# Optimization experiments

Hardware: AMD Instinct MI355X
Metric: run time of the kernel (lower is better)

The kernel has to match this reference:

```python
import jax, jax.numpy as jnp
import numpy as np

N_NODES = 10000
N_EDGES = 640000
D_FEAT = 128


def setup_inputs() -> dict:
    key = jax.random.key(0)
    k1, k2, k3 = jax.random.split(key, 3)
    feat = jax.random.normal(k1, (N_NODES, D_FEAT), dtype=jnp.float32)
    src = jax.random.randint(k2, (N_EDGES,), 0, N_NODES, dtype=jnp.int64)
    dst = jax.random.randint(k3, (N_EDGES,), 0, N_NODES, dtype=jnp.int64)
    beta = jnp.ones((1,), dtype=jnp.float32)
    return {"feat": feat, "src": src, "dst": dst, "beta": beta}


def reference(feat, src, dst, beta):
    # L2-normalize node features along feature dim (eps matches torch F.normalize)
    norm = feat / jnp.maximum(jnp.linalg.norm(feat, axis=-1, keepdims=True), 1e-12)
    # per-edge cosine similarity: sum over d of norm[src] * norm[dst]  -> [E]
    cos = jnp.einsum('ed,ed->e', norm[src], norm[dst])
    e = beta[0] * cos
    # edge softmax segmented over destination nodes
    seg_max = jax.ops.segment_max(e, dst, num_segments=N_NODES)  # [N]
    ex = jnp.exp(e - seg_max[dst])                               # [E]
    seg_sum = jax.ops.segment_sum(ex, dst, num_segments=N_NODES)  # [N]
    p = ex / seg_sum[dst]                                        # [E]
    # weighted neighbor aggregation: sum_e p_e * feat[src_e] into dst
    msg = feat[src] * p[:, None]                                 # [E, d]
    out = jax.ops.segment_sum(msg, dst, num_segments=N_NODES)    # [N, d]
    return out
```

## Files before the change

kernel.cpp:

```cpp
#include <hip/hip_runtime.h>
#include <math.h>

#define D_FEAT 128
#define EPB_SHIFT 12
#define EPB 4096
#define N_NODES_MAX 10016
#define CAP 128

__device__ __forceinline__ unsigned short f2bf(float x) {
    unsigned int b = __float_as_uint(x);
    return (unsigned short)((b + 0x7fffu + ((b >> 16) & 1u)) >> 16);
}
__device__ __forceinline__ float2 bf2_to_f2(unsigned int u) {
    return make_float2(__uint_as_float(u << 16), __uint_as_float(u & 0xffff0000u));
}

__global__ __launch_bounds__(1024) void hist_norm_kernel(
        const float* __restrict__ feat,
        const int* __restrict__ dst,
        unsigned int* __restrict__ nfb,
        float* __restrict__ invn,
        int* __restrict__ hist,
        unsigned short* __restrict__ lrank,
        int n_nodes, int n_edges, int nbh) {
    __shared__ int lhist[N_NODES_MAX];
    int tid = (int)threadIdx.x;
    if ((int)blockIdx.x < nbh) {
        int b = blockIdx.x;
        for (int i = tid; i < n_nodes; i += 1024) lhist[i] = 0;
        __syncthreads();
        int e0 = b << EPB_SHIFT;
        int e1 = e0 + EPB;
        if (e1 > n_edges) e1 = n_edges;
        for (int e = e0 + tid; e < e1; e += 1024) {
            int d = dst[e];
            lrank[e] = (unsigned short)atomicAdd(&lhist[d], 1);
        }
        __syncthreads();
        for (int i = tid; i < n_nodes; i += 1024)
            hist[b * n_nodes + i] = lhist[i];
    } else {
        int node = ((int)blockIdx.x - nbh) * 16 + (tid >> 6);
        int lane = tid & 63;
        if (node >= n_nodes) return;
        float2 f = ((const float2*)feat)[node * 64 + lane];
        float ss = f.x * f.x + f.y * f.y;
        #pragma unroll
        for (int off = 1; off < 64; off <<= 1)
            ss += __shfl_xor(ss, off, 64);
        unsigned int lo = f2bf(f.x), hi = f2bf(f.y);
        nfb[node * 64 + lane] = (hi << 16) | lo;
        if (lane == 0) invn[node] = 1.0f / fmaxf(sqrtf(ss), 1e-12f);
    }
}

__global__ __launch_bounds__(256) void scan_kernel(int* __restrict__ hist,
                                                   int* __restrict__ cnt,
                                                   int n_nodes, int nbh) {
    int node = (int)(blockIdx.x * blockDim.x + threadIdx.x);
    if (node >= n_nodes) return;
    int base = 0;
    #pragma unroll 8
    for (int b = 0; b < nbh; ++b) {
        int idx = b * n_nodes + node;
        int v = hist[idx];
        hist[idx] = base;
        base += v;
    }
    cnt[node] = base;
}

__global__ __launch_bounds__(256) void scatter_kernel(
        const int* __restrict__ src,
        const int* __restrict__ dst,
        const int* __restrict__ hist,
        const unsigned short* __restrict__ lrank,
        unsigned short* __restrict__ src_sorted,
        int n_nodes, int n_edges) {
    int e = blockIdx.x * blockDim.x + threadIdx.x;
    if (e >= n_edges) return;
    int d = dst[e];
    int b = e >> EPB_SHIFT;
    int r = hist[b * n_nodes + d] + (int)lrank[e];
    if (r < CAP)
        src_sorted[((size_t)d << 7) + r] = (unsigned short)src[e];
}

__global__ __launch_bounds__(256, 8) void agg_kernel(
        const unsigned int* __restrict__ nfb,
        const float* __restrict__ invn,
        const float* __restrict__ beta,
        const int* __restrict__ cnt,
        const unsigned short* __restrict__ src_sorted,
        float* __restrict__ out, int n_nodes) {
    int node = (int)(blockIdx.x * blockDim.x + threadIdx.x) >> 6;
    int lane = threadIdx.x & 63;
    if (node >= n_nodes) return;
    int deg = cnt[node];
    if (deg > CAP) deg = CAP;
    int beg = node << 7;
    int end = beg + deg;
    int q  = lane >> 4;
    int ql = lane & 15;
    float bd = beta[0] * invn[node];

    uint4 du = ((const uint4*)nfb)[(size_t)node * 16 + ql];
    float2 d0 = bf2_to_f2(du.x), d1 = bf2_to_f2(du.y);
    float2 d2 = bf2_to_f2(du.z), d3 = bf2_to_f2(du.w);

    float l = 0.0f;
    float a0 = 0.f, a1 = 0.f, a2 = 0.f, a3 = 0.f;
    float a4 = 0.f, a5 = 0.f, a6 = 0.f, a7 = 0.f;

    for (int base = beg; base < end; base += 64) {
        int nb = end - base;
        if (nb > 64) nb = 64;
        int idx = (int)src_sorted[base + lane];

        #pragma unroll 8
        for (int j = 0; j < nb; j += 4) {
            int jj = j + q;
            bool v = jj < nb;
            int sj = __shfl(idx, jj, 64);
            sj = v ? sj : 0;
            uint4 u = ((const uint4*)nfb)[(size_t)sj * 16 + ql];
            float ivj = invn[sj];
            float2 f0 = bf2_to_f2(u.x), f1 = bf2_to_f2(u.y);
            float2 f2 = bf2_to_f2(u.z), f3 = bf2_to_f2(u.w);
            float part = f0.x * d0.x + f0.y * d0.y + f1.x * d1.x + f1.y * d1.y
                       + f2.x * d2.x + f2.y * d2.y + f3.x * d3.x + f3.y * d3.y;
            part += __shfl_xor(part, 1, 64);
            part += __shfl_xor(part, 2, 64);
            part += __shfl_xor(part, 4, 64);
            part += __shfl_xor(part, 8, 64);
            float w = v ? __expf(part * ivj * bd) : 0.0f;
            l += w;
            a0 += w * f0.x;  a1 += w * f0.y;
            a2 += w * f1.x;  a3 += w * f1.y;
            a4 += w * f2.x;  a5 += w * f2.y;
            a6 += w * f3.x;  a7 += w * f3.y;
        }
    }
    #pragma unroll
    for (int off = 1; off < 64; off <<= 1)
        l += __shfl_xor(l, off, 64);
    a0 += __shfl_xor(a0, 16, 64); a0 += __shfl_xor(a0, 32, 64);
    a1 += __shfl_xor(a1, 16, 64); a1 += __shfl_xor(a1, 32, 64);
    a2 += __shfl_xor(a2, 16, 64); a2 += __shfl_xor(a2, 32, 64);
    a3 += __shfl_xor(a3, 16, 64); a3 += __shfl_xor(a3, 32, 64);
    a4 += __shfl_xor(a4, 16, 64); a4 += __shfl_xor(a4, 32, 64);
    a5 += __shfl_xor(a5, 16, 64); a5 += __shfl_xor(a5, 32, 64);
    a6 += __shfl_xor(a6, 16, 64); a6 += __shfl_xor(a6, 32, 64);
    a7 += __shfl_xor(a7, 16, 64); a7 += __shfl_xor(a7, 32, 64);
    float invl = (l > 0.0f) ? (16.0f / l) : 0.0f;
    if (q == 0) {
        float4* o = (float4*)out + (size_t)node * 32 + ql * 2;
        o[0] = make_float4(a0 * invl, a1 * invl, a2 * invl, a3 * invl);
        o[1] = make_float4(a4 * invl, a5 * invl, a6 * invl, a7 * invl);
    }
}

extern "C" void kernel_launch(void* const* d_in, const int* in_sizes, int n_in,
                              void* d_out, int out_size, void* d_ws, size_t ws_size,
                              hipStream_t stream) {
    const float* feat = (const float*)d_in[0];
    const int* src    = (const int*)d_in[1];
    const int* dst    = (const int*)d_in[2];
    const float* beta = (const float*)d_in[3];
    float* out = (float*)d_out;

    const int n_nodes = in_sizes[0] / D_FEAT;
    const int n_edges = in_sizes[1];
    const int nbh = (n_edges + EPB - 1) >> EPB_SHIFT;

    char* ws = (char*)d_ws;
    size_t off = 0;
    auto alloc = [&](size_t bytes) -> void* {
        void* p = ws + off;
        off += (bytes + 255) & ~(size_t)255;
        return p;
    };
    unsigned int*   nfb        = (unsigned int*)alloc((size_t)n_nodes * 64 * 4);
    float*          invn       = (float*)alloc((size_t)n_nodes * 4);
    int*            hist       = (int*)  alloc((size_t)nbh * n_nodes * 4);
    int*            cnt        = (int*)  alloc((size_t)n_nodes * 4);
    unsigned short* lrank      = (unsigned short*)alloc((size_t)n_edges * 2);
    unsigned short* src_sorted = (unsigned short*)alloc((size_t)n_nodes * CAP * 2);

    int nb_norm = (n_nodes + 15) / 16;
    hist_norm_kernel<<<nbh + nb_norm, 1024, 0, stream>>>(
        feat, dst, nfb, invn, hist, lrank, n_nodes, n_edges, nbh);

    scan_kernel<<<(n_nodes + 255) / 256, 256, 0, stream>>>(hist, cnt, n_nodes, nbh);

    scatter_kernel<<<(n_edges + 255) / 256, 256, 0, stream>>>(
        src, dst, hist, lrank, src_sorted, n_nodes, n_edges);

    agg_kernel<<<(n_nodes + 3) / 4, 256, 0, stream>>>(
        nfb, invn, beta, cnt, src_sorted, out, n_nodes);
}
```

Measured before the change: 126.5 us.

## Use DPP row reductions, preload per-chunk norms, and enlarge histogram blocks

Replaces the four cross-lane shuffle reductions in the aggregation inner loop with DPP row operations (quad permutes plus half-mirror and mirror) so the 16-lane dot-product sum stays within a row. Each chunk now loads the source inverse-norm times beta once per lane and broadcasts it by shuffle, instead of issuing a scattered invn load per edge. It also doubles edges per histogram block, halving the number of per-block histograms the scan must walk, and drops the launch_bounds occupancy hint. Mirror-based reductions leave lanes holding the correct total only if the mirrored sums are symmetric, which they are for a full sum, and larger blocks reduce hist-stage parallelism.

```diff
diff --git a/kernel.cpp b/kernel.cpp
--- a/kernel.cpp
+++ b/kernel.cpp
@@ -2,10 +2,15 @@
 #include <math.h>
 
 #define D_FEAT 128
-#define EPB_SHIFT 12
-#define EPB 4096
+#define EPB_SHIFT 13
+#define EPB 8192
 #define N_NODES_MAX 10016
 #define CAP 128
+
+#define DPP_XOR1 0xB1
+#define DPP_XOR2 0x4E
+#define DPP_HALF_MIRROR 0x141
+#define DPP_MIRROR      0x140
 
 __device__ __forceinline__ unsigned short f2bf(float x) {
     unsigned int b = __float_as_uint(x);
@@ -13,6 +18,12 @@
 }
 __device__ __forceinline__ float2 bf2_to_f2(unsigned int u) {
     return make_float2(__uint_as_float(u << 16), __uint_as_float(u & 0xffff0000u));
+}
+template <int CTRL>
+__device__ __forceinline__ float dpp_add(float x) {
+    int t = __builtin_amdgcn_update_dpp(__float_as_int(x), __float_as_int(x),
+                                        CTRL, 0xF, 0xF, false);
+    return x + __int_as_float(t);
 }
 
 __global__ __launch_bounds__(1024) void hist_norm_kernel(
@@ -86,13 +97,12 @@
         src_sorted[((size_t)d << 7) + r] = (unsigned short)src[e];
 }
 
-__global__ __launch_bounds__(256, 8) void agg_kernel(
-        const unsigned int* __restrict__ nfb,
-        const float* __restrict__ invn,
-        const float* __restrict__ beta,
-        const int* __restrict__ cnt,
-        const unsigned short* __restrict__ src_sorted,
-        float* __restrict__ out, int n_nodes) {
+__global__ void agg_kernel(const unsigned int* __restrict__ nfb,
+                           const float* __restrict__ invn,
+                           const float* __restrict__ beta,
+                           const int* __restrict__ cnt,
+                           const unsigned short* __restrict__ src_sorted,
+                           float* __restrict__ out, int n_nodes) {
     int node = (int)(blockIdx.x * blockDim.x + threadIdx.x) >> 6;
     int lane = threadIdx.x & 63;
     if (node >= n_nodes) return;
@@ -115,25 +125,27 @@
     for (int base = beg; base < end; base += 64) {
         int nb = end - base;
         if (nb > 64) nb = 64;
-        int idx = (int)src_sorted[base + lane];
+        int gi = base + lane;
+        bool valid = gi < end;
+        int idx = valid ? (int)src_sorted[gi] : 0;
+        float ivm = valid ? invn[idx] * bd : 0.0f;
 
         #pragma unroll 8
         for (int j = 0; j < nb; j += 4) {
             int jj = j + q;
-            bool v = jj < nb;
-            int sj = __shfl(idx, jj, 64);
-            sj = v ? sj : 0;
+            int   sj  = __shfl(idx, jj, 64);
+            float inj = __shfl(ivm, jj, 64);
             uint4 u = ((const uint4*)nfb)[(size_t)sj * 16 + ql];
-            float ivj = invn[sj];
             float2 f0 = bf2_to_f2(u.x), f1 = bf2_to_f2(u.y);
             float2 f2 = bf2_to_f2(u.z), f3 = bf2_to_f2(u.w);
             float part = f0.x * d0.x + f0.y * d0.y + f1.x * d1.x + f1.y * d1.y
                        + f2.x * d2.x + f2.y * d2.y + f3.x * d3.x + f3.y * d3.y;
-            part += __shfl_xor(part, 1, 64);
-            part += __shfl_xor(part, 2, 64);
-            part += __shfl_xor(part, 4, 64);
-            part += __shfl_xor(part, 8, 64);
-            float w = v ? __expf(part * ivj * bd) : 0.0f;
+            part = dpp_add<DPP_XOR1>(part);
+            part = dpp_add<DPP_XOR2>(part);
+            part = dpp_add<DPP_HALF_MIRROR>(part);
+            part = dpp_add<DPP_MIRROR>(part);
+            float w = __expf(part * inj);
+            w = (jj < nb) ? w : 0.0f;
             l += w;
             a0 += w * f0.x;  a1 += w * f0.y;
             a2 += w * f1.x;  a3 += w * f1.y;
```

Result: faster. 112.9 us (-10.8%).
